# Kernel optimization log

Hardware: AMD Instinct MI355X
Metric: run time of the kernel (lower is better)

The kernel has to match this reference:

```python
import jax, jax.numpy as jnp
import numpy as np

EMBED = 1024
HEADS = 16
HEAD_DIM = EMBED // HEADS


def setup_inputs() -> dict:
    key = jax.random.key(0)
    ks = jax.random.split(key, 6)
    B, T, C = 4, 2048, EMBED
    x = jax.random.normal(ks[0], (B, T, C), dtype=jnp.float32)
    # random binary mask [B,1,1,T]; keep at least one valid key per row by forcing first position to 1
    mask = jax.random.randint(ks[1], (B, 1, 1, T), 0, 2, dtype=jnp.int32)
    mask = mask.at[..., 0].set(1)
    scale = 1.0 / np.sqrt(C)
    qkv_w = jax.random.normal(ks[2], (3 * C, C), dtype=jnp.float32) * scale  # torch Linear weight [out,in]
    qkv_b = jax.random.normal(ks[3], (3 * C,), dtype=jnp.float32) * scale
    out_w = jax.random.normal(ks[4], (C, C), dtype=jnp.float32) * scale
    out_b = jax.random.normal(ks[5], (C,), dtype=jnp.float32) * scale
    return {"x": x, "mask": mask, "qkv_w": qkv_w, "qkv_b": qkv_b, "out_w": out_w, "out_b": out_b}


def reference(x, mask, qkv_w, qkv_b, out_w, out_b):
    B, T, C = x.shape
    H, D = HEADS, HEAD_DIM
    qkv = x @ qkv_w.T + qkv_b  # [B,T,3C]
    qkv = qkv.reshape(B, T, 3, H, D).transpose(2, 0, 3, 1, 4)  # [3,B,H,T,D]
    q, k, v = qkv[0], qkv[1], qkv[2]
    scores = jnp.einsum('bhqd,bhkd->bhqk', q, k) / np.sqrt(D)
    scores = jnp.where(mask == 0, -jnp.inf, scores)
    attn = jax.nn.softmax(scores, axis=-1)
    out = jnp.einsum('bhqk,bhkd->bhqd', attn, v)
    out = out.transpose(0, 2, 1, 3).reshape(B, T, C)
    return out @ out_w.T + out_b
```

## Files before the change

kernel.cpp:

```cpp
#include <hip/hip_runtime.h>
#include <hip/hip_bf16.h>

typedef _Float16 f16;
typedef _Float16 f16x4_t __attribute__((ext_vector_type(4)));
typedef _Float16 f16x8 __attribute__((ext_vector_type(8)));
typedef float f32x4 __attribute__((ext_vector_type(4)));

#define AS1(p) ((const __attribute__((address_space(1))) void*)(p))
#define AS3(p) ((__attribute__((address_space(3))) void*)(p))

__device__ __forceinline__ void gload_lds16(const f16* g, f16* l) {
    __builtin_amdgcn_global_load_lds(AS1(g), AS3(l), 16, 0, 0);
}

__device__ __forceinline__ f16x8 cvt8(float4 u, float4 v) {
    f16x8 r;
    r[0] = (f16)u.x; r[1] = (f16)u.y; r[2] = (f16)u.z; r[3] = (f16)u.w;
    r[4] = (f16)v.x; r[5] = (f16)v.y; r[6] = (f16)v.z; r[7] = (f16)v.w;
    return r;
}

#define Q_SCALE 0.180336880111f

__global__ __launch_bounds__(256) void pre_pass(
    const float* __restrict__ x, const float* __restrict__ qw,
    const int* __restrict__ mask, f16* __restrict__ x16,
    f16* __restrict__ w16, int* __restrict__ gpos, int* __restrict__ nkv)
{
    const int blk = blockIdx.x;
    if (blk >= 2048) {
        const int b = blk - 2048;
        if (threadIdx.x < 64) {
            const int lane = threadIdx.x;
            const int* mb = mask + b * 2048;
            int run = 0;
            for (int c = 0; c < 2048; c += 64) {
                int v = (mb[c + lane] != 0) ? 1 : 0;
                unsigned long long bits = __ballot(v);
                int pre = __popcll(bits & ((1ull << lane) - 1ull));
                if (v) gpos[b * 2048 + run + pre] = c + lane;
                run += __popcll(bits);
            }
            if (lane == 0) nkv[b] = run;
        }
        return;
    }
    const int nx8 = 8192 * 1024 / 8;
    const int nw8 = 3072 * 1024 / 8;
    int idx = blk * 256 + threadIdx.x;
    const int stride = 2048 * 256;
    for (int i = idx; i < nx8 + nw8; i += stride) {
        const float* s; f16* d;
        if (i < nx8) { size_t o = (size_t)i * 8;          s = x  + o; d = x16 + o; }
        else         { size_t o = (size_t)(i - nx8) * 8;  s = qw + o; d = w16 + o; }
        float4 u = *(const float4*)s;
        float4 v = *(const float4*)(s + 4);
        *(f16x8*)d = cvt8(u, v);
    }
}

__global__ __launch_bounds__(256) void cvt_f32_f16(
    const float* __restrict__ src, f16* __restrict__ dst, int n8)
{
    int idx = blockIdx.x * 256 + threadIdx.x;
    int stride = gridDim.x * 256;
    for (int i = idx; i < n8; i += stride) {
        size_t o = (size_t)i * 8;
        float4 u = *(const float4*)&src[o];
        float4 v = *(const float4*)&src[o + 4];
        *(f16x8*)&dst[o] = cvt8(u, v);
    }
}

__global__ __launch_bounds__(256) void gemm_qkv_f16(
    const f16* __restrict__ x16, const f16* __restrict__ w16,
    const float* __restrict__ bias, const int* __restrict__ gpos,
    const int* __restrict__ nkv, f16* __restrict__ q_g,
    f16* __restrict__ k_g, f16* __restrict__ vt_g)
{
    constexpr int BK = 64, K = 1024, NT = K / BK;
    __shared__ f16 As[2][128 * BK], Bs[2][128 * BK];

    const int tid  = threadIdx.x;
    const int lane = tid & 63, wave = tid >> 6;
    const int wy = wave >> 1, wx = wave & 1;
    const int lrow = lane & 15, quad = lane >> 4;
    const int srow = lane >> 3;
    const int sgrp = lane & 7;
    const int x0 = ((quad)     ^ (lrow & 7)) * 8;
    const int x1 = ((4 + quad) ^ (lrow & 7)) * 8;

    const int bx = blockIdx.x, by = blockIdx.y;
    const int z = (bx >= 8);
    int b_kv = 0, mt = 0, nk = 0, nbase, n0;
    if (!z) {
        nbase = 0; n0 = bx * 128;
    } else {
        b_kv = by >> 4; mt = by & 15;
        nk = nkv[b_kv];
        if (mt * 128 >= nk) return;
        nbase = 1024; n0 = (bx - 8) * 128;
    }

    const f16* arow[4];
    const f16* brow[4];
#pragma unroll
    for (int j = 0; j < 4; ++j) {
        int rit = (wave * 4 + j) * 8 + srow;
        int trow;
        if (!z) {
            trow = by * 128 + rit;
        } else {
            int ct = mt * 128 + rit;
            int t = (ct < nk) ? gpos[b_kv * 2048 + ct] : 0;
            trow = b_kv * 2048 + t;
        }
        arow[j] = x16 + (size_t)trow * K + (sgrp ^ srow) * 8;
        brow[j] = w16 + (size_t)(nbase + n0 + rit) * K + (sgrp ^ srow) * 8;
    }

    auto stage = [&](int k0, int bsel) {
#pragma unroll
        for (int j = 0; j < 4; ++j) {
            int rg = wave * 4 + j;
            gload_lds16(arow[j] + k0, &As[bsel][rg * 512 + lane * 8]);
            gload_lds16(brow[j] + k0, &Bs[bsel][rg * 512 + lane * 8]);
        }
    };

    f32x4 acc[4][4] = {};

    stage(0, 0);
    stage(BK, 1);
    asm volatile("s_waitcnt vmcnt(8)" ::: "memory");
    __builtin_amdgcn_s_barrier();

    for (int kt = 0; kt < NT; ++kt) {
        const int cur = kt & 1;

        f16x8 a0[4], a1[4], b0[4], b1[4];
#pragma unroll
        for (int i = 0; i < 4; ++i) {
            const int r = (wy * 64 + i * 16 + lrow) * BK;
            a0[i] = *(const f16x8*)&As[cur][r + x0];
            a1[i] = *(const f16x8*)&As[cur][r + x1];
        }
#pragma unroll
        for (int j = 0; j < 4; ++j) {
            const int r = (wx * 64 + j * 16 + lrow) * BK;
            b0[j] = *(const f16x8*)&Bs[cur][r + x0];
            b1[j] = *(const f16x8*)&Bs[cur][r + x1];
        }
        __builtin_amdgcn_s_setprio(1);
#pragma unroll
        for (int i = 0; i < 4; ++i)
#pragma unroll
            for (int j = 0; j < 4; ++j) {
                acc[i][j] = __builtin_amdgcn_mfma_f32_16x16x32_f16(a0[i], b0[j], acc[i][j], 0, 0, 0);
                acc[i][j] = __builtin_amdgcn_mfma_f32_16x16x32_f16(a1[i], b1[j], acc[i][j], 0, 0, 0);
            }
        __builtin_amdgcn_s_setprio(0);

        __builtin_amdgcn_s_barrier();
        if (kt + 2 < NT) {
            stage((kt + 2) * BK, cur);
            asm volatile("s_waitcnt vmcnt(8)" ::: "memory");
        } else {
            asm volatile("s_waitcnt vmcnt(0)" ::: "memory");
        }
        __builtin_amdgcn_s_barrier();
    }

    if (!z) {
#pragma unroll
        for (int i = 0; i < 4; ++i) {
            size_t row = (size_t)by * 128 + wy * 64 + i * 16 + quad * 4;
            int b = (int)(row >> 11);
            int t = (int)(row & 2047);
#pragma unroll
            for (int j = 0; j < 4; ++j) {
                int col = n0 + wx * 64 + j * 16 + lrow;
                float bb = bias[col];
                int hh = col >> 6, d = col & 63;
                size_t o = ((size_t)(b * 16 + hh) * 2048 + t) * 64 + d;
#pragma unroll
                for (int r = 0; r < 4; ++r)
                    q_g[o + (size_t)r * 64] = (f16)((acc[i][j][r] + bb) * Q_SCALE);
            }
        }
    } else {
        const int region = n0 >> 10;
#pragma unroll
        for (int i = 0; i < 4; ++i) {
            int ct = mt * 128 + wy * 64 + i * 16 + quad * 4;
#pragma unroll
            for (int j = 0; j < 4; ++j) {
                int col = n0 + wx * 64 + j * 16 + lrow;
                float bb = bias[1024 + col];
                int cl = col & 1023, hh = cl >> 6, d = cl & 63;
                size_t bh = (size_t)(b_kv * 16 + hh);
                if (region == 0) {
#pragma unroll
                    for (int r = 0; r < 4; ++r)
                        k_g[(bh * 2048 + ct + r) * 64 + d] = (f16)(acc[i][j][r] + bb);
                } else {
                    f16x4_t pv;
#pragma unroll
                    for (int r = 0; r < 4; ++r) pv[r] = (f16)(acc[i][j][r] + bb);
                    *(f16x4_t*)&vt_g[(bh * 64 + d) * 2048 + ct] = pv;
                }
            }
        }
    }
}

__global__ __launch_bounds__(256) void gemm2_f16(
    const f16* __restrict__ A16, const f16* __restrict__ Bw16,
    const float* __restrict__ bias, float* __restrict__ C,
    int M, int N, int K)
{
    constexpr int BK = 64;
    __shared__ f16 As[2][128 * BK], Bs[2][128 * BK];

    const int tid  = threadIdx.x;
    const int lane = tid & 63, wave = tid >> 6;
    const int wy = wave >> 1, wx = wave & 1;
    const int lrow = lane & 15, quad = lane >> 4;
    const size_t m0 = (size_t)blockIdx.y * 128;
    const size_t n0 = (size_t)blockIdx.x * 128;
    const int srow = lane >> 3, sgrp = lane & 7;
    const int x0 = ((quad)     ^ (lrow & 7)) * 8;
    const int x1 = ((4 + quad) ^ (lrow & 7)) * 8;

    const f16* arow[4];
    const f16* brow[4];
#pragma unroll
    for (int j = 0; j < 4; ++j) {
        int rit = (wave * 4 + j) * 8 + srow;
        arow[j] = A16  + (m0 + rit) * (size_t)K + (sgrp ^ srow) * 8;
        brow[j] = Bw16 + (n0 + rit) * (size_t)K + (sgrp ^ srow) * 8;
    }

    auto stage = [&](int k0, int bsel) {
#pragma unroll
        for (int j = 0; j < 4; ++j) {
            int rg = wave * 4 + j;
            gload_lds16(arow[j] + k0, &As[bsel][rg * 512 + lane * 8]);
            gload_lds16(brow[j] + k0, &Bs[bsel][rg * 512 + lane * 8]);
        }
    };

    f32x4 acc[4][4] = {};
    const int NT = K / BK;

    stage(0, 0);
    stage(BK, 1);
    asm volatile("s_waitcnt vmcnt(8)" ::: "memory");
    __builtin_amdgcn_s_barrier();

    for (int kt = 0; kt < NT; ++kt) {
        const int cur = kt & 1;

        f16x8 a0[4], a1[4], b0[4], b1[4];
#pragma unroll
        for (int i = 0; i < 4; ++i) {
            const int r = (wy * 64 + i * 16 + lrow) * BK;
            a0[i] = *(const f16x8*)&As[cur][r + x0];
            a1[i] = *(const f16x8*)&As[cur][r + x1];
        }
#pragma unroll
        for (int j = 0; j < 4; ++j) {
            const int r = (wx * 64 + j * 16 + lrow) * BK;
            b0[j] = *(const f16x8*)&Bs[cur][r + x0];
            b1[j] = *(const f16x8*)&Bs[cur][r + x1];
        }
        __builtin_amdgcn_s_setprio(1);
#pragma unroll
        for (int i = 0; i < 4; ++i)
#pragma unroll
            for (int j = 0; j < 4; ++j) {
                acc[i][j] = __builtin_amdgcn_mfma_f32_16x16x32_f16(a0[i], b0[j], acc[i][j], 0, 0, 0);
                acc[i][j] = __builtin_amdgcn_mfma_f32_16x16x32_f16(a1[i], b1[j], acc[i][j], 0, 0, 0);
            }
        __builtin_amdgcn_s_setprio(0);

        __builtin_amdgcn_s_barrier();
        if (kt + 2 < NT) {
            stage((kt + 2) * BK, cur);
            asm volatile("s_waitcnt vmcnt(8)" ::: "memory");
        } else {
            asm volatile("s_waitcnt vmcnt(0)" ::: "memory");
        }
        __builtin_amdgcn_s_barrier();
    }

#pragma unroll
    for (int i = 0; i < 4; ++i) {
        size_t row = m0 + wy * 64 + i * 16 + quad * 4;
#pragma unroll
        for (int j = 0; j < 4; ++j) {
            size_t col = n0 + wx * 64 + j * 16 + lrow;
            float bb = bias[col];
#pragma unroll
            for (int r = 0; r < 4; ++r)
                C[(row + r) * N + col] = acc[i][j][r] + bb;
        }
    }
}

__global__ __launch_bounds__(256) void attn_f16(
    const f16* __restrict__ q_g, const f16* __restrict__ k_g,
    const f16* __restrict__ vt_g, const int* __restrict__ nkv,
    f16* __restrict__ att, int B, int T)
{
    constexpr int LDP = 72;
    __shared__ f16 Ks_s[2][64 * 64];
    __shared__ f16 Vt_s[2][64 * 64];
    __shared__ f16 Pt[128 * LDP];

    const int tid  = threadIdx.x;
    const int lane = tid & 63, wave = tid >> 6;
    const int lrow = lane & 15, quad = lane >> 4;
    const int bid = ((int)blockIdx.x & 7) * 128 + ((int)blockIdx.x >> 3);
    const int qt = bid & 15;
    const int h  = (bid >> 4) & 15;
    const int b  = bid >> 8;
    const size_t base = (size_t)b * T;
    const size_t bh = (size_t)(b * 16 + h);
    const f16* qg_base = q_g  + bh * (2048 * 64);
    const f16* kg_base = k_g  + bh * (2048 * 64);
    const f16* vt_base = vt_g + bh * (64 * 2048);

    const int nk = nkv[b];
    const int ntiles = (nk + 63) >> 6;

    const int x0 = ((quad)     ^ (lrow & 7)) * 8;
    const int x1 = ((4 + quad) ^ (lrow & 7)) * 8;

    f16x8 aq[2][2];
#pragma unroll
    for (int qi = 0; qi < 2; ++qi)
#pragma unroll
        for (int ks = 0; ks < 2; ++ks)
            aq[qi][ks] = *(const f16x8*)&qg_base[
                (size_t)(qt * 128 + wave * 32 + qi * 16 + lrow) * 64 + ks * 32 + quad * 8];

    f32x4 oacc[2][4] = {};
    float l_part[2] = {0.f, 0.f};

    const int srow0 = (lane >> 3);
    const int sgrp  = (lane & 7);

    auto stage = [&](int kt, int bsel) {
        const f16* kT = kg_base + kt * 4096;
#pragma unroll
        for (int j = 0; j < 2; ++j) {
            int rg  = wave + j * 4;
            int row = rg * 8 + srow0;
            int grp = sgrp ^ (row & 7);
            gload_lds16(&kT[row * 64 + grp * 8], &Ks_s[bsel][rg * 512 + lane * 8]);
            gload_lds16(&vt_base[(size_t)row * 2048 + kt * 64 + grp * 8],
                        &Vt_s[bsel][rg * 512 + lane * 8]);
        }
    };

    stage(0, 0);
    stage(1, 1);
    asm volatile("s_waitcnt vmcnt(4)" ::: "memory");
    __builtin_amdgcn_s_barrier();

    for (int kt = 0; kt < ntiles; ++kt) {
        const int cur = kt & 1;
        const f16* Ks = Ks_s[cur];
        const f16* Vt = Vt_s[cur];

        f32x4 s[2][4];
        __builtin_amdgcn_s_setprio(1);
#pragma unroll
        for (int ni = 0; ni < 4; ++ni) {
            const int key = ni * 16 + lrow;
            f16x8 k0 = *(const f16x8*)&Ks[key * 64 + x0];
            f16x8 k1 = *(const f16x8*)&Ks[key * 64 + x1];
#pragma unroll
            for (int qi = 0; qi < 2; ++qi) {
                f32x4 t = {0.f, 0.f, 0.f, 0.f};
                t = __builtin_amdgcn_mfma_f32_16x16x32_f16(k0, aq[qi][0], t, 0, 0, 0);
                t = __builtin_amdgcn_mfma_f32_16x16x32_f16(k1, aq[qi][1], t, 0, 0, 0);
                s[qi][ni] = t;
            }
        }
        __builtin_amdgcn_s_setprio(0);

        const int rem = nk - kt * 64;
        auto softmax = [&](bool masked) {
#pragma unroll
            for (int qi = 0; qi < 2; ++qi)
#pragma unroll
                for (int ni = 0; ni < 4; ++ni) {
                    float p[4];
#pragma unroll
                    for (int r = 0; r < 4; ++r) {
                        float e = __builtin_amdgcn_exp2f(s[qi][ni][r]);
                        p[r] = (!masked || (ni * 16 + quad * 4 + r) < rem) ? e : 0.f;
                    }
                    l_part[qi] += (p[0] + p[1]) + (p[2] + p[3]);
                    f16x4_t pk;
#pragma unroll
                    for (int r = 0; r < 4; ++r) pk[r] = (f16)p[r];
                    *(f16x4_t*)&Pt[(wave * 32 + qi * 16 + lrow) * LDP + ni * 16 + quad * 4] = pk;
                }
        };
        if (rem >= 64) softmax(false); else softmax(true);

        f16x8 pf[2][2];
#pragma unroll
        for (int qi = 0; qi < 2; ++qi)
#pragma unroll
            for (int ks = 0; ks < 2; ++ks)
                pf[qi][ks] = *(const f16x8*)&Pt[(wave * 32 + qi * 16 + lrow) * LDP + ks * 32 + quad * 8];
        __builtin_amdgcn_s_setprio(1);
#pragma unroll
        for (int di = 0; di < 4; ++di) {
            const int d = di * 16 + lrow;
            f16x8 v0 = *(const f16x8*)&Vt[d * 64 + x0];
            f16x8 v1 = *(const f16x8*)&Vt[d * 64 + x1];
#pragma unroll
            for (int qi = 0; qi < 2; ++qi) {
                oacc[qi][di] = __builtin_amdgcn_mfma_f32_16x16x32_f16(v0, pf[qi][0], oacc[qi][di], 0, 0, 0);
                oacc[qi][di] = __builtin_amdgcn_mfma_f32_16x16x32_f16(v1, pf[qi][1], oacc[qi][di], 0, 0, 0);
            }
        }
        __builtin_amdgcn_s_setprio(0);

        __builtin_amdgcn_s_barrier();
        if (kt + 2 < ntiles) {
            stage(kt + 2, cur);
            asm volatile("s_waitcnt vmcnt(4)" ::: "memory");
        } else {
            asm volatile("s_waitcnt vmcnt(0)" ::: "memory");
        }
        __builtin_amdgcn_s_barrier();
    }

#pragma unroll
    for (int qi = 0; qi < 2; ++qi) {
        float v = l_part[qi];
        v += __shfl_xor(v, 16);
        v += __shfl_xor(v, 32);
        float inv = 1.f / v;
        int q = qt * 128 + wave * 32 + qi * 16 + lrow;
#pragma unroll
        for (int di = 0; di < 4; ++di) {
            f16x4_t o;
#pragma unroll
            for (int r = 0; r < 4; ++r) o[r] = (f16)(oacc[qi][di][r] * inv);
            *(f16x4_t*)&att[(base + q) * 1024 + h * 64 + di * 16 + quad * 4] = o;
        }
    }
}

extern "C" void kernel_launch(void* const* d_in, const int* in_sizes, int n_in,
                              void* d_out, int out_size, void* d_ws, size_t ws_size,
                              hipStream_t stream) {
    const float* x     = (const float*)d_in[0];
    const int*   mask  = (const int*)d_in[1];
    const float* qkv_w = (const float*)d_in[2];
    const float* qkv_b = (const float*)d_in[3];
    const float* out_w = (const float*)d_in[4];
    const float* out_b = (const float*)d_in[5];
    float* out = (float*)d_out;

    const int B = 4, T = 2048;
    const int M = B * T;
    char* ws = (char*)d_ws;
    f16* q_g = (f16*)(ws);
    f16* k_g = (f16*)(ws + 16777216);
    f16* vt  = (f16*)(ws + 33554432);
    f16* att = (f16*)(ws + 50331648);

    f16* x16 = (f16*)d_out;
    f16* w16 = (f16*)((char*)d_out + 16777216);
    int* gpos = (int*)((char*)d_out + 23068672);
    int* nkv  = gpos + 4 * 2048;
    f16* ow16 = q_g;

    dim3 blk(256);
    pre_pass<<<dim3(2052), blk, 0, stream>>>(x, qkv_w, mask, x16, w16, gpos, nkv);
    gemm_qkv_f16<<<dim3(24, 64), blk, 0, stream>>>(x16, w16, qkv_b, gpos, nkv, q_g, k_g, vt);
    attn_f16<<<dim3(B * 16 * 16), blk, 0, stream>>>(q_g, k_g, vt, nkv, att, B, T);
    cvt_f32_f16<<<dim3(512), blk, 0, stream>>>(out_w, ow16, 1024 * 1024 / 8);
    gemm2_f16<<<dim3(1024 / 128, M / 128), blk, 0, stream>>>(att, ow16, out_b, out, M, 1024, 1024);
}
```

Before: 253.4 us.

## Fuse out_w fp32-to-fp16 conversion into output projection GEMM B-tile loading

```diff
diff --git a/kernel.cpp b/kernel.cpp
--- a/kernel.cpp
+++ b/kernel.cpp
@@ -59,19 +59,6 @@
     }
 }
 
-__global__ __launch_bounds__(256) void cvt_f32_f16(
-    const float* __restrict__ src, f16* __restrict__ dst, int n8)
-{
-    int idx = blockIdx.x * 256 + threadIdx.x;
-    int stride = gridDim.x * 256;
-    for (int i = idx; i < n8; i += stride) {
-        size_t o = (size_t)i * 8;
-        float4 u = *(const float4*)&src[o];
-        float4 v = *(const float4*)&src[o + 4];
-        *(f16x8*)&dst[o] = cvt8(u, v);
-    }
-}
-
 __global__ __launch_bounds__(256) void gemm_qkv_f16(
     const f16* __restrict__ x16, const f16* __restrict__ w16,
     const float* __restrict__ bias, const int* __restrict__ gpos,
@@ -215,7 +202,7 @@
 }
 
 __global__ __launch_bounds__(256) void gemm2_f16(
-    const f16* __restrict__ A16, const f16* __restrict__ Bw16,
+    const f16* __restrict__ A16, const float* __restrict__ Bw,
     const float* __restrict__ bias, float* __restrict__ C,
     int M, int N, int K)
 {
@@ -233,33 +220,51 @@
     const int x1 = ((4 + quad) ^ (lrow & 7)) * 8;
 
     const f16* arow[4];
-    const f16* brow[4];
 #pragma unroll
     for (int j = 0; j < 4; ++j) {
         int rit = (wave * 4 + j) * 8 + srow;
-        arow[j] = A16  + (m0 + rit) * (size_t)K + (sgrp ^ srow) * 8;
-        brow[j] = Bw16 + (n0 + rit) * (size_t)K + (sgrp ^ srow) * 8;
-    }
-
-    auto stage = [&](int k0, int bsel) {
-#pragma unroll
-        for (int j = 0; j < 4; ++j) {
-            int rg = wave * 4 + j;
-            gload_lds16(arow[j] + k0, &As[bsel][rg * 512 + lane * 8]);
-            gload_lds16(brow[j] + k0, &Bs[bsel][rg * 512 + lane * 8]);
+        arow[j] = A16 + (m0 + rit) * (size_t)K + (sgrp ^ srow) * 8;
+    }
+    const int rB = tid >> 1;
+    const int hB = (tid & 1) * 32;
+    const float* bsrc = Bw + (n0 + rB) * (size_t)K + hB;
+
+    auto stageA = [&](int k0, int bsel) {
+#pragma unroll
+        for (int j = 0; j < 4; ++j)
+            gload_lds16(arow[j] + k0, &As[bsel][(wave * 4 + j) * 512 + lane * 8]);
+    };
+
+    float4 regs[8];
+    auto loadB = [&](int k0) {
+#pragma unroll
+        for (int t = 0; t < 8; ++t)
+            regs[t] = *(const float4*)(bsrc + k0 + t * 4);
+    };
+    auto writeB = [&](int bsel) {
+#pragma unroll
+        for (int g = 0; g < 4; ++g) {
+            f16x8 v = cvt8(regs[2 * g], regs[2 * g + 1]);
+            int grp = (hB >> 3) + g;
+            int swz = grp ^ (rB & 7);
+            *(f16x8*)&Bs[bsel][rB * 64 + swz * 8] = v;
         }
     };
 
     f32x4 acc[4][4] = {};
     const int NT = K / BK;
 
-    stage(0, 0);
-    stage(BK, 1);
-    asm volatile("s_waitcnt vmcnt(8)" ::: "memory");
-    __builtin_amdgcn_s_barrier();
+    loadB(0);
+    stageA(0, 0);
+    writeB(0);
+    __syncthreads();
 
     for (int kt = 0; kt < NT; ++kt) {
         const int cur = kt & 1;
+        if (kt + 1 < NT) {
+            loadB((kt + 1) * BK);
+            stageA((kt + 1) * BK, cur ^ 1);
+        }
 
         f16x8 a0[4], a1[4], b0[4], b1[4];
 #pragma unroll
@@ -284,14 +289,8 @@
             }
         __builtin_amdgcn_s_setprio(0);
 
-        __builtin_amdgcn_s_barrier();
-        if (kt + 2 < NT) {
-            stage((kt + 2) * BK, cur);
-            asm volatile("s_waitcnt vmcnt(8)" ::: "memory");
-        } else {
-            asm volatile("s_waitcnt vmcnt(0)" ::: "memory");
-        }
-        __builtin_amdgcn_s_barrier();
+        if (kt + 1 < NT) writeB(cur ^ 1);
+        __syncthreads();
     }
 
 #pragma unroll
@@ -482,12 +481,10 @@
     f16* w16 = (f16*)((char*)d_out + 16777216);
     int* gpos = (int*)((char*)d_out + 23068672);
     int* nkv  = gpos + 4 * 2048;
-    f16* ow16 = q_g;
 
     dim3 blk(256);
     pre_pass<<<dim3(2052), blk, 0, stream>>>(x, qkv_w, mask, x16, w16, gpos, nkv);
     gemm_qkv_f16<<<dim3(24, 64), blk, 0, stream>>>(x16, w16, qkv_b, gpos, nkv, q_g, k_g, vt);
     attn_f16<<<dim3(B * 16 * 16), blk, 0, stream>>>(q_g, k_g, vt, nkv, att, B, T);
-    cvt_f32_f16<<<dim3(512), blk, 0, stream>>>(out_w, ow16, 1024 * 1024 / 8);
-    gemm2_f16<<<dim3(1024 / 128, M / 128), blk, 0, stream>>>(att, ow16, out_b, out, M, 1024, 1024);
-}
+    gemm2_f16<<<dim3(1024 / 128, M / 128), blk, 0, stream>>>(att, out_w, out_b, out, M, 1024, 1024);
+}
```

Result: slower. 269.9 us (+6.5%).
